# Kernel optimization log

Hardware: AMD Instinct MI355X
Metric: run time of the kernel (lower is better)

Reference implementation:

```python
import jax, jax.numpy as jnp
import numpy as np

B, D, H, W, C = 1, 16, 56, 56, 256
WD, WH, WW = 2, 7, 7
SD, SH, SW = 1, 3, 3
HEADS = 8
HDIM = C // HEADS
N = WD * WH * WW          # 98 tokens per window
NW = (D // WD) * (H // WH) * (W // WW)  # 512 windows per batch element
HID = 4 * C


def _rel_index():
    coords = np.stack(np.meshgrid(np.arange(WD), np.arange(WH), np.arange(WW), indexing='ij')).reshape(3, -1)
    rel = (coords[:, :, None] - coords[:, None, :]).transpose(1, 2, 0).astype(np.int64)
    rel[..., 0] += WD - 1; rel[..., 1] += WH - 1; rel[..., 2] += WW - 1
    rel[..., 0] *= (2 * WH - 1) * (2 * WW - 1)
    rel[..., 1] *= (2 * WW - 1)
    return rel.sum(-1)  # (N, N)

REL_INDEX = jnp.asarray(_rel_index())


def _np_window_partition(x):
    b, d, h, w, c = x.shape
    x = x.reshape(b, d // WD, WD, h // WH, WH, w // WW, WW, c)
    return x.transpose(0, 1, 3, 5, 2, 4, 6, 7).reshape(-1, N, c)


def _compute_mask():
    # Swin compute_mask: label 3x3x3 shifted regions, windows mask cross-region pairs with -100
    img = np.zeros((1, D, H, W, 1), np.float32)
    cnt = 0
    for ds in (slice(0, -WD), slice(-WD, -SD), slice(-SD, None)):
        for hs in (slice(0, -WH), slice(-WH, -SH), slice(-SH, None)):
            for ws in (slice(0, -WW), slice(-WW, -SW), slice(-SW, None)):
                img[:, ds, hs, ws, :] = cnt; cnt += 1
    mw = _np_window_partition(img).reshape(NW, N)
    am = mw[:, None, :] - mw[:, :, None]
    return np.where(am != 0, -100.0, 0.0).astype(np.float32)


def setup_inputs():
    key = jax.random.key(0)
    ks = jax.random.split(key, 8)
    s = 0.02
    return {
        'x': jax.random.normal(ks[0], (B, D, H, W, C), jnp.float32),
        'mask_matrix': jnp.asarray(_compute_mask()),
        'g1': jnp.ones((C,), jnp.float32), 'b1': jnp.zeros((C,), jnp.float32),
        'qkv_w': jax.random.normal(ks[1], (C, 3 * C), jnp.float32) * s,
        'qkv_b': jnp.zeros((3 * C,), jnp.float32),
        'rpb': jax.random.normal(ks[2], ((2 * WD - 1) * (2 * WH - 1) * (2 * WW - 1), HEADS), jnp.float32) * s,
        'proj_w': jax.random.normal(ks[3], (C, C), jnp.float32) * s,
        'proj_b': jnp.zeros((C,), jnp.float32),
        'g2': jnp.ones((C,), jnp.float32), 'b2': jnp.zeros((C,), jnp.float32),
        'fc1_w': jax.random.normal(ks[4], (C, HID), jnp.float32) * s,
        'fc1_b': jnp.zeros((HID,), jnp.float32),
        'fc2_w': jax.random.normal(ks[5], (HID, C), jnp.float32) * s,
        'fc2_b': jnp.zeros((C,), jnp.float32),
    }


def _ln(x, g, b):
    mu = jnp.mean(x, -1, keepdims=True)
    var = jnp.mean((x - mu) ** 2, -1, keepdims=True)
    return (x - mu) * jax.lax.rsqrt(var + 1e-5) * g + b


def _window_partition(x):
    b = x.shape[0]
    x = x.reshape(b, D // WD, WD, H // WH, WH, W // WW, WW, C)
    return x.transpose(0, 1, 3, 5, 2, 4, 6, 7).reshape(-1, N, C)


def _window_reverse(w):
    x = w.reshape(B, D // WD, H // WH, W // WW, WD, WH, WW, C)
    return x.transpose(0, 1, 4, 2, 5, 3, 6, 7).reshape(B, D, H, W, C)


def reference(x, mask_matrix, g1, b1, qkv_w, qkv_b, rpb, proj_w, proj_b, g2, b2, fc1_w, fc1_b, fc2_w, fc2_b):
    shortcut = x
    y = _ln(x, g1, b1)
    # D,H,W divide window sizes -> pad amounts are 0; cyclic shift for SW-MSA
    y = jnp.roll(y, shift=(-SD, -SH, -SW), axis=(1, 2, 3))
    xw = _window_partition(y)                          # (B_, N, C)
    B_ = xw.shape[0]
    qkv = (xw @ qkv_w + qkv_b).reshape(B_, N, 3, HEADS, HDIM)
    q, k, v = jnp.moveaxis(qkv, 2, 0)                  # each (B_, N, HEADS, HDIM)
    q = q * (HDIM ** -0.5)
    attn = jnp.einsum('bnhd,bmhd->bhnm', q, k)         # (B_, HEADS, N, N)
    bias = rpb[REL_INDEX.reshape(-1)].reshape(N, N, HEADS).transpose(2, 0, 1)
    attn = attn + bias[None]
    attn = attn.reshape(B_ // NW, NW, HEADS, N, N) + mask_matrix[None, :, None]
    attn = jax.nn.softmax(attn.reshape(B_, HEADS, N, N), axis=-1)
    out = jnp.einsum('bhnm,bmhd->bnhd', attn, v).reshape(B_, N, C)
    out = out @ proj_w + proj_b
    y = _window_reverse(out)
    y = jnp.roll(y, shift=(SD, SH, SW), axis=(1, 2, 3))
    x = shortcut + y
    h = _ln(x, g2, b2)
    h = jax.nn.gelu(h @ fc1_w + fc1_b, approximate=False)
    h = h @ fc2_w + fc2_b
    return x + h
```

## Files before the change

kernel.cpp:

```cpp
#include <hip/hip_runtime.h>
#include <hip/hip_bf16.h>

typedef __hip_bfloat16 bf16;
typedef __attribute__((ext_vector_type(4))) float f32x4;
typedef __attribute__((ext_vector_type(8))) short bf16x8;

#define MFMA16(a,b,c) __builtin_amdgcn_mfma_f32_16x16x32_bf16((a),(b),(c),0,0,0)

static __device__ inline unsigned short bfbits(float f) {
  __hip_bfloat16 h = __float2bfloat16(f);
  union { __hip_bfloat16 h; unsigned short u; } u;
  u.h = h; return u.u;
}
static __device__ inline float bf2f(unsigned short u) {
  return __uint_as_float(((unsigned int)u) << 16);
}
static __device__ inline void gld16(const void* g, void* l) {
  __builtin_amdgcn_global_load_lds((const __attribute__((address_space(1))) void*)g,
                                   (__attribute__((address_space(3))) void*)l, 16, 0, 0);
}

__global__ __launch_bounds__(256) void prep_k(const float* __restrict__ qkv_w,
                                              const float* __restrict__ proj_w,
                                              const float* __restrict__ fc1_w,
                                              const float* __restrict__ fc2_w,
                                              const float* __restrict__ rpb,
                                              bf16* __restrict__ wqkvT,
                                              bf16* __restrict__ wprojT,
                                              bf16* __restrict__ wfc1T,
                                              bf16* __restrict__ wfc2T,
                                              unsigned short* __restrict__ biasT,
                                              unsigned int* __restrict__ rowoff0,
                                              unsigned int* __restrict__ rowmap1) {
  const int b = blockIdx.x, tid = threadIdx.x;
  if (b < 768) {
    int idx = b * 256 + tid;
    int n = idx >> 8, k = idx & 255;
    float v = qkv_w[k * 768 + n];
    if (n < 256) v *= 0.17677669529663687f;
    wqkvT[idx] = __float2bfloat16(v);
  } else if (b < 1024) {
    int idx = (b - 768) * 256 + tid;
    int n = idx >> 8, k = idx & 255;
    wprojT[idx] = __float2bfloat16(proj_w[k * 256 + n]);
  } else if (b < 2048) {
    int idx = (b - 1024) * 256 + tid;
    int n = idx >> 8, k = idx & 255;
    wfc1T[idx] = __float2bfloat16(fc1_w[k * 1024 + n]);
  } else if (b < 3072) {
    int idx = (b - 2048) * 256 + tid;
    int n = idx >> 10, k = idx & 1023;
    wfc2T[idx] = __float2bfloat16(fc2_w[k * 256 + n]);
  } else if (b < 3110) {
    int idx = (b - 3072) * 256 + tid;
    if (idx < 9604) {
      int nn = idx / 98, mm = idx - nn * 98;
      int ld = nn / 49, lrem = nn - ld * 49, lh = lrem / 7, lw = lrem - lh * 7;
      int md = mm / 49, mrem = mm - md * 49, mh = mrem / 7, mw = mrem - mh * 7;
      int rel = (ld - md + 1) * 169 + (lh - mh + 6) * 13 + (lw - mw + 6);
      #pragma unroll
      for (int h = 0; h < 8; ++h)
        biasT[h * 9604 + mm * 98 + nn] = bfbits(rpb[rel * 8 + h]);
    }
  } else {
    int row = (b - 3110) * 256 + tid;
    if (row < 50176) {
      int widx = row / 98, n = row - widx * 98;
      rowoff0[row] = (unsigned int)(widx * 25088 + n * 32);
      int zd = widx >> 6, zh = (widx >> 3) & 7, zw = widx & 7;
      int ld = n / 49, rem = n - ld * 49, lh = rem / 7, lw = rem - lh * 7;
      int d = zd * 2 + ld, h = zh * 7 + lh, w = zw * 7 + lw;
      int dsrc = (d + 1) & 15;
      int hsrc = h + 3; if (hsrc >= 56) hsrc -= 56;
      int wsrc = w + 3; if (wsrc >= 56) wsrc -= 56;
      rowmap1[row] = (unsigned int)((dsrc * 56 + hsrc) * 56 + wsrc);
    }
  }
}

__global__ __launch_bounds__(256) void vtrans_k(const unsigned short* __restrict__ v,
                                                unsigned short* __restrict__ vt) {
  __shared__ unsigned short S[98 * 33];
  const unsigned short* src = v + (size_t)blockIdx.x * 3136;
  for (int i = threadIdx.x; i < 3136; i += 256) {
    int n = i >> 5, d = i & 31;
    S[n * 33 + d] = src[i];
  }
  __syncthreads();
  unsigned short* dst = vt + ((size_t)blockIdx.x << 12);
  for (int i = threadIdx.x; i < 4096; i += 256) {
    int d = i >> 7, m = i & 127;
    dst[i] = (m < 98) ? S[m * 33 + d] : (unsigned short)0;
  }
}

__global__ __launch_bounds__(256) void ln_k(const float* __restrict__ x,
                                            const float* __restrict__ g,
                                            const float* __restrict__ bias,
                                            bf16* __restrict__ out, int windowed) {
  const int wid = threadIdx.x >> 6, lane = threadIdx.x & 63;
  const int t = blockIdx.x * 4 + wid;
  int src = t;
  if (windowed) {
    int widx = t / 98, n = t - widx * 98;
    int zd = widx >> 6, zh = (widx >> 3) & 7, zw = widx & 7;
    int ld = n / 49, rem = n - ld * 49, lh = rem / 7, lw = rem - lh * 7;
    int d = zd * 2 + ld, h = zh * 7 + lh, w = zw * 7 + lw;
    int dsrc = (d + 1) & 15;
    int hsrc = h + 3; if (hsrc >= 56) hsrc -= 56;
    int wsrc = w + 3; if (wsrc >= 56) wsrc -= 56;
    src = (dsrc * 56 + hsrc) * 56 + wsrc;
  }
  const float4 v = *(const float4*)(x + (size_t)src * 256 + lane * 4);
  float s1 = v.x + v.y + v.z + v.w;
  float s2 = v.x * v.x + v.y * v.y + v.z * v.z + v.w * v.w;
  #pragma unroll
  for (int d = 1; d < 64; d <<= 1) {
    s1 += __shfl_xor(s1, d);
    s2 += __shfl_xor(s2, d);
  }
  float mu = s1 * (1.f / 256.f);
  float var = s2 * (1.f / 256.f) - mu * mu;
  float rs = rsqrtf(var + 1e-5f);
  const float4 gv = *(const float4*)(g + lane * 4);
  const float4 bv = *(const float4*)(bias + lane * 4);
  ushort4 pk;
  pk.x = bfbits((v.x - mu) * rs * gv.x + bv.x);
  pk.y = bfbits((v.y - mu) * rs * gv.y + bv.y);
  pk.z = bfbits((v.z - mu) * rs * gv.z + bv.z);
  pk.w = bfbits((v.w - mu) * rs * gv.w + bv.w);
  *(ushort4*)((unsigned short*)out + (size_t)t * 256 + lane * 4) = pk;
}

template<int EPI>
__global__ __launch_bounds__(512) void gemm_k(const bf16* __restrict__ A,
                                              const bf16* __restrict__ Bt,
                                              const float* __restrict__ bias,
                                              int N, int K, int NX, int mrow0,
                                              bf16* __restrict__ out_bf,
                                              float* __restrict__ out_f,
                                              const float* __restrict__ add_f,
                                              const unsigned int* __restrict__ rmap) {
  __shared__ bf16 As[2][128 * 32];
  __shared__ bf16 Bs[2][256 * 32];
  const int tid = threadIdx.x;
  const int wid = tid >> 6, lane = tid & 63;
  const int nwg = gridDim.x, xcd = blockIdx.x & 7, o8 = blockIdx.x >> 3;
  const int qq = nwg >> 3, r8 = nwg & 7;
  const int tile = (xcd < r8 ? xcd * (qq + 1) : r8 * (qq + 1) + (xcd - r8) * qq) + o8;
  const int bx = tile % NX, by = tile / NX;
  const int row0 = by * 128, col0 = bx * 256;
  const int fr = lane & 15, kh = lane >> 4;
  const int wm = (wid >> 2) * 64, wn = (wid & 3) * 64;
  f32x4 zero4 = {0.f, 0.f, 0.f, 0.f};
  f32x4 acc[4][4];
  #pragma unroll
  for (int i = 0; i < 4; ++i)
    #pragma unroll
    for (int j = 0; j < 4; ++j) acc[i][j] = zero4;

  const int srow = tid >> 2, sq = (tid & 3) * 8;
  const bf16* aP = A + (size_t)(row0 + srow) * K + sq;
  const bf16* bP = Bt + (size_t)(col0 + srow) * K + sq;
  const bf16* bP2 = Bt + (size_t)(col0 + srow + 128) * K + sq;
  bf16* asD = &As[0][srow * 32 + sq];
  bf16* bsD = &Bs[0][srow * 32 + sq];
  bf16* bsD2 = &Bs[0][(srow + 128) * 32 + sq];

  const int nk = K >> 5;
  gld16(aP, asD);
  gld16(bP, bsD);
  gld16(bP2, bsD2);

  int cur = 0;
  for (int t = 0; t < nk; ++t) {
    __syncthreads();
    if (t + 1 < nk) {
      int k0 = (t + 1) * 32;
      int so = (cur ^ 1);
      gld16(aP + k0, asD + so * 4096);
      gld16(bP + k0, bsD + so * 8192);
      gld16(bP2 + k0, bsD2 + so * 8192);
    }
    const bf16* Ab = As[cur];
    const bf16* Bb = Bs[cur];
    bf16x8 af[4], bfr[4];
    #pragma unroll
    for (int i = 0; i < 4; ++i)
      af[i] = *(const bf16x8*)&Ab[(wm + i * 16 + fr) * 32 + kh * 8];
    #pragma unroll
    for (int j = 0; j < 4; ++j)
      bfr[j] = *(const bf16x8*)&Bb[(wn + j * 16 + fr) * 32 + kh * 8];
    #pragma unroll
    for (int i = 0; i < 4; ++i)
      #pragma unroll
      for (int j = 0; j < 4; ++j)
        acc[i][j] = MFMA16(af[i], bfr[j], acc[i][j]);
    cur ^= 1;
  }

  #pragma unroll
  for (int i = 0; i < 4; ++i) {
    #pragma unroll
    for (int r = 0; r < 4; ++r) {
      int row = row0 + wm + i * 16 + kh * 4 + r;
      unsigned int rl = (EPI == 0 || EPI == 1) ? rmap[row] : 0u;
      #pragma unroll
      for (int j = 0; j < 4; ++j) {
        int col = col0 + wn + j * 16 + fr;
        float bb = bias[col];
        if (EPI == 0 && col < 256) bb *= 0.17677669529663687f;
        float v = acc[i][j][r] + bb;
        if (EPI == 0) {
          int part = col >> 8, head = (col >> 5) & 7, hd = col & 31;
          size_t off = (size_t)part * 12845056 + rl + head * 3136 + hd;
          out_bf[off] = __float2bfloat16(v);
        } else if (EPI == 1) {
          size_t tok = rl;
          out_f[tok * 256 + col] = add_f[tok * 256 + col] + v;
        } else if (EPI == 2) {
          float gl = 0.5f * v * (1.0f + erff(v * 0.70710678118654752f));
          out_bf[(size_t)row * 1024 + col] = __float2bfloat16(gl);
        } else {
          size_t ro = (size_t)(mrow0 + row);
          out_f[ro * 256 + col] = add_f[ro * 256 + col] + v;
        }
      }
    }
  }
}

__global__ __launch_bounds__(256, 2) void attn_k(const bf16* __restrict__ qkv,
                                                 const unsigned short* __restrict__ vt,
                                                 const unsigned short* __restrict__ bias_bf,
                                                 bf16* __restrict__ out) {
  __shared__ unsigned short Pl[112 * 128];
  __shared__ unsigned short biasS[112 * 100];
  __shared__ float invS[112];
  __shared__ unsigned char lblS[112];
  const int tid = threadIdx.x;
  const int widx = blockIdx.x >> 1, hh = blockIdx.x & 1;
  const int wid = tid >> 6, lane = tid & 63;
  const int fr = lane & 15, kh = lane >> 4, kh4 = kh * 4;
  const int tr0 = wid * 2;
  f32x4 zero4 = {0.f, 0.f, 0.f, 0.f};

  if (tid < 112) {
    unsigned char l = 255;
    if (tid < 98) {
      int zd = widx >> 6, zh = (widx >> 3) & 7, zw = widx & 7;
      int ld = tid / 49, rem = tid - ld * 49, lh = rem / 7, lw = rem - lh * 7;
      int d = zd * 2 + ld, h = zh * 7 + lh, w = zw * 7 + lw;
      int cd = (d >= 14) + (d >= 15);
      int ch = (h >= 49) + (h >= 53);
      int cw = (w >= 49) + (w >= 53);
      l = (unsigned char)(cd * 9 + ch * 3 + cw);
    }
    lblS[tid] = l;
  }
  __syncthreads();

  unsigned int lblK[7];
  #pragma unroll
  for (int mt = 0; mt < 7; ++mt)
    lblK[mt] = *(const unsigned int*)&lblS[mt * 16 + kh4];
  const bool t1v = (tr0 + 1) < 7;
  unsigned int lq0 = 0x01010101u * lblS[tr0 * 16 + fr];
  unsigned int lq1 = 0x01010101u * lblS[(t1v ? tr0 + 1 : 0) * 16 + fr];

  for (int it = 0; it < 4; ++it) {
    const int head = hh * 4 + it;
    const unsigned short* qbu = (const unsigned short*)qkv + ((size_t)widx * 8 + head) * 3136;
    const unsigned short* kbu = qbu + (size_t)12845056;
    const unsigned short* brow = bias_bf + head * 9604;
    const unsigned short* vtb = vt + (((size_t)widx * 8 + head) << 12);

    __syncthreads();
    for (int j = tid; j < 4802; j += 256) {
      int n = j / 49, m2 = (j - n * 49) * 2;
      *(unsigned int*)&biasS[n * 100 + m2] = *(const unsigned int*)(brow + n * 98 + m2);
    }
    for (int j = tid; j < 700; j += 256) {
      int n = j / 50, m2 = (j - n * 50) * 2;
      *(unsigned int*)&biasS[(98 + n) * 100 + m2] = 0xFF80FF80u;
    }

    int qr0 = tr0 * 16 + fr; if (qr0 > 97) qr0 = 97;
    int qr1 = (tr0 + 1) * 16 + fr; if (qr1 > 97) qr1 = 97;
    bf16x8 aq0 = *(const bf16x8*)(qbu + qr0 * 32 + kh * 8);
    bf16x8 aq1 = *(const bf16x8*)(qbu + qr1 * 32 + kh * 8);

    f32x4 s2[2][7];
    #pragma unroll
    for (int a = 0; a < 2; ++a)
      #pragma unroll
      for (int m = 0; m < 7; ++m) s2[a][m] = zero4;
    #pragma unroll
    for (int mt = 0; mt < 7; ++mt) {
      int krow = mt * 16 + fr; if (krow > 97) krow = 97;
      bf16x8 kf = *(const bf16x8*)(kbu + krow * 32 + kh * 8);
      s2[0][mt] = MFMA16(kf, aq0, s2[0][mt]);
      s2[1][mt] = MFMA16(kf, aq1, s2[1][mt]);
    }
    __syncthreads();

    #pragma unroll
    for (int ti = 0; ti < 2; ++ti) {
      int tr = tr0 + ti;
      if (tr < 7) {
        int q = tr * 16 + fr;
        int qc = (q < 98) ? q : 0;
        unsigned int lq = (ti == 0) ? lq0 : lq1;
        float mxa = -1e30f, mxb = -1e30f;
        #pragma unroll
        for (int mt = 0; mt < 7; ++mt) {
          unsigned int df = lblK[mt] ^ lq;
          #pragma unroll
          for (int r = 0; r < 4; ++r) {
            int k = mt * 16 + kh4 + r;
            float b = bf2f(biasS[k * 100 + qc]);
            float msk = ((df >> (8 * r)) & 255u) ? -100.f : 0.f;
            s2[ti][mt][r] = s2[ti][mt][r] + b + msk;
          }
          mxa = fmaxf(mxa, fmaxf(s2[ti][mt][0], s2[ti][mt][1]));
          mxb = fmaxf(mxb, fmaxf(s2[ti][mt][2], s2[ti][mt][3]));
        }
        float mx = fmaxf(mxa, mxb);
        mx = fmaxf(mx, __shfl_xor(mx, 16));
        mx = fmaxf(mx, __shfl_xor(mx, 32));
        float suma = 0.f, sumb = 0.f;
        #pragma unroll
        for (int mt = 0; mt < 7; ++mt) {
          float e0 = __expf(s2[ti][mt][0] - mx);
          float e1 = __expf(s2[ti][mt][1] - mx);
          float e2 = __expf(s2[ti][mt][2] - mx);
          float e3 = __expf(s2[ti][mt][3] - mx);
          s2[ti][mt][0] = e0; s2[ti][mt][1] = e1;
          s2[ti][mt][2] = e2; s2[ti][mt][3] = e3;
          suma += e0 + e1; sumb += e2 + e3;
        }
        float sum = suma + sumb;
        sum += __shfl_xor(sum, 16);
        sum += __shfl_xor(sum, 32);
        if (kh == 0) invS[q] = 1.0f / sum;
        #pragma unroll
        for (int mt = 0; mt < 7; ++mt) {
          ushort4 pk;
          pk.x = bfbits(s2[ti][mt][0]);
          pk.y = bfbits(s2[ti][mt][1]);
          pk.z = bfbits(s2[ti][mt][2]);
          pk.w = bfbits(s2[ti][mt][3]);
          *(ushort4*)&Pl[(q * 128 + mt * 16 + kh4) ^ ((q & 7) << 3)] = pk;
        }
        ushort4 zz; zz.x = zz.y = zz.z = zz.w = 0;
        *(ushort4*)&Pl[(q * 128 + 112 + kh4) ^ ((q & 7) << 3)] = zz;
      }
    }

    f32x4 o00 = zero4, o01 = zero4, o10 = zero4, o11 = zero4;
    #pragma unroll
    for (int kk = 0; kk < 4; ++kk) {
      bf16x8 vv0 = *(const bf16x8*)(vtb + fr * 128 + kk * 32 + kh * 8);
      bf16x8 vv1 = *(const bf16x8*)(vtb + (16 + fr) * 128 + kk * 32 + kh * 8);
      int prow0 = tr0 * 16 + fr;
      bf16x8 pa0 = *(const bf16x8*)&((const bf16*)Pl)[(prow0 * 128 + kk * 32 + kh * 8) ^ ((prow0 & 7) << 3)];
      o00 = MFMA16(pa0, vv0, o00);
      o01 = MFMA16(pa0, vv1, o01);
      if (t1v) {
        int prow1 = prow0 + 16;
        bf16x8 pa1 = *(const bf16x8*)&((const bf16*)Pl)[(prow1 * 128 + kk * 32 + kh * 8) ^ ((prow1 & 7) << 3)];
        o10 = MFMA16(pa1, vv0, o10);
        o11 = MFMA16(pa1, vv1, o11);
      }
    }
    #pragma unroll
    for (int r = 0; r < 4; ++r) {
      int row = tr0 * 16 + kh4 + r;
      if (row < 98) {
        float iv = invS[row];
        size_t grow = (size_t)widx * 98 + row;
        out[grow * 256 + head * 32 + fr] = __float2bfloat16(o00[r] * iv);
        out[grow * 256 + head * 32 + 16 + fr] = __float2bfloat16(o01[r] * iv);
      }
    }
    if (t1v) {
      #pragma unroll
      for (int r = 0; r < 4; ++r) {
        int row = (tr0 + 1) * 16 + kh4 + r;
        if (row < 98) {
          float iv = invS[row];
          size_t grow = (size_t)widx * 98 + row;
          out[grow * 256 + head * 32 + fr] = __float2bfloat16(o10[r] * iv);
          out[grow * 256 + head * 32 + 16 + fr] = __float2bfloat16(o11[r] * iv);
        }
      }
    }
  }
}

extern "C" void kernel_launch(void* const* d_in, const int* in_sizes, int n_in,
                              void* d_out, int out_size, void* d_ws, size_t ws_size,
                              hipStream_t stream) {
  const float* x      = (const float*)d_in[0];
  const float* g1     = (const float*)d_in[2];
  const float* b1     = (const float*)d_in[3];
  const float* qkv_w  = (const float*)d_in[4];
  const float* qkv_b  = (const float*)d_in[5];
  const float* rpb    = (const float*)d_in[6];
  const float* proj_w = (const float*)d_in[7];
  const float* proj_b = (const float*)d_in[8];
  const float* g2     = (const float*)d_in[9];
  const float* b2     = (const float*)d_in[10];
  const float* fc1_w  = (const float*)d_in[11];
  const float* fc1_b  = (const float*)d_in[12];
  const float* fc2_w  = (const float*)d_in[13];
  const float* fc2_b  = (const float*)d_in[14];
  float* outp = (float*)d_out;

  char* ws = (char*)d_ws;
  if (ws_size < (size_t)156237824) return;
  bf16*  wqkvT   = (bf16*)(ws + 0);
  bf16*  wprojT  = (bf16*)(ws + 393216);
  bf16*  wfc1T   = (bf16*)(ws + 524288);
  bf16*  wfc2T   = (bf16*)(ws + 1048576);
  unsigned short* bias_bf = (unsigned short*)(ws + 1572864);
  unsigned int* rowmap1 = (unsigned int*)(ws + 1726528);
  float* x2      = (float*)(ws + 2097152);
  unsigned int* rowoff0 = (unsigned int*)(ws + 2097152);
  unsigned short* vtb = (unsigned short*)(ws + 11931648);
  char*  pool    = ws + 53477376;
  bf16*  xw       = (bf16*)pool;
  bf16*  qkvb     = (bf16*)(pool + 25690112);
  bf16*  attn_out = (bf16*)pool;
  bf16*  hbuf     = (bf16*)pool;
  bf16*  hh       = (bf16*)(pool + 25690112);

  prep_k<<<3307, 256, 0, stream>>>(qkv_w, proj_w, fc1_w, fc2_w, rpb,
                                   wqkvT, wprojT, wfc1T, wfc2T, bias_bf,
                                   rowoff0, rowmap1);

  ln_k<<<12544, 256, 0, stream>>>(x, g1, b1, xw, 1);
  gemm_k<0><<<1176, 512, 0, stream>>>(xw, wqkvT, qkv_b, 768, 256, 3, 0,
                                      qkvb, nullptr, nullptr, rowoff0);
  vtrans_k<<<4096, 256, 0, stream>>>((const unsigned short*)qkvb + (size_t)2 * 12845056, vtb);
  attn_k<<<1024, 256, 0, stream>>>(qkvb, vtb, bias_bf, attn_out);
  gemm_k<1><<<392, 512, 0, stream>>>(attn_out, wprojT, proj_b, 256, 256, 1, 0,
                                     nullptr, x2, x, rowmap1);
  ln_k<<<12544, 256, 0, stream>>>(x2, g2, b2, hbuf, 0);
  for (int ch = 0; ch < 2; ++ch) {
    gemm_k<2><<<784, 512, 0, stream>>>(hbuf + (size_t)ch * 25088 * 256, wfc1T, fc1_b,
                                       1024, 256, 4, 0, hh, nullptr, nullptr, nullptr);
    gemm_k<3><<<196, 512, 0, stream>>>(hh, wfc2T, fc2_b, 256, 1024, 1, ch * 25088,
                                       nullptr, outp, x2, nullptr);
  }
}
```

Baseline: 307.1 us.

## Fuse MLP fc1+GELU+fc2 into one kernel keeping hidden tile in LDS

```diff
diff --git a/kernel.cpp b/kernel.cpp
--- a/kernel.cpp
+++ b/kernel.cpp
@@ -203,7 +203,7 @@
   for (int i = 0; i < 4; ++i) {
     #pragma unroll
     for (int r = 0; r < 4; ++r) {
-      int row = row0 + wm + i * 16 + kh * 4 + r;
+      int row = row0 + wm + i * 16 + (lane >> 4) * 4 + r;
       unsigned int rl = (EPI == 0 || EPI == 1) ? rmap[row] : 0u;
       #pragma unroll
       for (int j = 0; j < 4; ++j) {
@@ -218,13 +218,126 @@
         } else if (EPI == 1) {
           size_t tok = rl;
           out_f[tok * 256 + col] = add_f[tok * 256 + col] + v;
-        } else if (EPI == 2) {
+        }
+      }
+    }
+  }
+}
+
+__global__ __launch_bounds__(256) void mlp_k(const bf16* __restrict__ hbuf,
+                                             const bf16* __restrict__ w1,
+                                             const bf16* __restrict__ w2,
+                                             const float* __restrict__ b1,
+                                             const float* __restrict__ b2,
+                                             const float* __restrict__ x2,
+                                             float* __restrict__ out) {
+  __shared__ bf16 Ah[64 * 256];
+  __shared__ bf16 Hh[64 * 256];
+  const int tid = threadIdx.x;
+  const int wid = tid >> 6, lane = tid & 63;
+  const int fr = lane & 15, kh = lane >> 4, kh4 = kh * 4;
+  const int wn = wid * 64;
+  const int row0 = blockIdx.x * 64;
+  f32x4 zero4 = {0.f, 0.f, 0.f, 0.f};
+
+  {
+    int row = tid >> 2, cg = (tid & 3) * 64;
+    const bf16* src = hbuf + (size_t)(row0 + row) * 256 + cg;
+    #pragma unroll
+    for (int c = 0; c < 8; ++c) {
+      bf16x8 v = *(const bf16x8*)(src + c * 8);
+      *(bf16x8*)&Ah[(row * 256 + cg + c * 8) ^ ((row & 7) << 3)] = v;
+    }
+  }
+  __syncthreads();
+
+  f32x4 acc2[4][4];
+  #pragma unroll
+  for (int i = 0; i < 4; ++i)
+    #pragma unroll
+    for (int j = 0; j < 4; ++j) acc2[i][j] = zero4;
+
+  for (int p = 0; p < 4; ++p) {
+    f32x4 acc1[4][4];
+    #pragma unroll
+    for (int i = 0; i < 4; ++i)
+      #pragma unroll
+      for (int j = 0; j < 4; ++j) acc1[i][j] = zero4;
+    const bf16* w1p = w1 + (size_t)(p * 256 + wn) * 256;
+    bf16x8 bcur[4], bnxt[4];
+    #pragma unroll
+    for (int j = 0; j < 4; ++j)
+      bcur[j] = *(const bf16x8*)(w1p + (j * 16 + fr) * 256 + kh * 8);
+    #pragma unroll
+    for (int t = 0; t < 8; ++t) {
+      if (t < 7) {
+        #pragma unroll
+        for (int j = 0; j < 4; ++j)
+          bnxt[j] = *(const bf16x8*)(w1p + (j * 16 + fr) * 256 + (t + 1) * 32 + kh * 8);
+      }
+      bf16x8 af[4];
+      #pragma unroll
+      for (int i = 0; i < 4; ++i)
+        af[i] = *(const bf16x8*)&Ah[((i * 16 + fr) * 256 + t * 32 + kh * 8) ^ ((fr & 7) << 3)];
+      #pragma unroll
+      for (int i = 0; i < 4; ++i)
+        #pragma unroll
+        for (int j = 0; j < 4; ++j)
+          acc1[i][j] = MFMA16(af[i], bcur[j], acc1[i][j]);
+      #pragma unroll
+      for (int j = 0; j < 4; ++j) bcur[j] = bnxt[j];
+    }
+    __syncthreads();
+    #pragma unroll
+    for (int j = 0; j < 4; ++j) {
+      float b1v = b1[p * 256 + wn + j * 16 + fr];
+      #pragma unroll
+      for (int i = 0; i < 4; ++i) {
+        #pragma unroll
+        for (int r = 0; r < 4; ++r) {
+          float v = acc1[i][j][r] + b1v;
           float gl = 0.5f * v * (1.0f + erff(v * 0.70710678118654752f));
-          out_bf[(size_t)row * 1024 + col] = __float2bfloat16(gl);
-        } else {
-          size_t ro = (size_t)(mrow0 + row);
-          out_f[ro * 256 + col] = add_f[ro * 256 + col] + v;
+          int row = i * 16 + kh4 + r;
+          Hh[(row * 256 + wn + j * 16 + fr) ^ ((row & 7) << 3)] = __float2bfloat16(gl);
         }
+      }
+    }
+    __syncthreads();
+    const bf16* w2p = w2 + p * 256;
+    bf16x8 c2[4], n2[4];
+    #pragma unroll
+    for (int j = 0; j < 4; ++j)
+      c2[j] = *(const bf16x8*)(w2p + (size_t)(wn + j * 16 + fr) * 1024 + kh * 8);
+    #pragma unroll
+    for (int t = 0; t < 8; ++t) {
+      if (t < 7) {
+        #pragma unroll
+        for (int j = 0; j < 4; ++j)
+          n2[j] = *(const bf16x8*)(w2p + (size_t)(wn + j * 16 + fr) * 1024 + (t + 1) * 32 + kh * 8);
+      }
+      bf16x8 hf[4];
+      #pragma unroll
+      for (int i = 0; i < 4; ++i)
+        hf[i] = *(const bf16x8*)&Hh[((i * 16 + fr) * 256 + t * 32 + kh * 8) ^ ((fr & 7) << 3)];
+      #pragma unroll
+      for (int i = 0; i < 4; ++i)
+        #pragma unroll
+        for (int j = 0; j < 4; ++j)
+          acc2[i][j] = MFMA16(hf[i], c2[j], acc2[i][j]);
+      #pragma unroll
+      for (int j = 0; j < 4; ++j) c2[j] = n2[j];
+    }
+  }
+
+  #pragma unroll
+  for (int i = 0; i < 4; ++i) {
+    #pragma unroll
+    for (int r = 0; r < 4; ++r) {
+      size_t row = (size_t)row0 + i * 16 + kh4 + r;
+      #pragma unroll
+      for (int j = 0; j < 4; ++j) {
+        int col = wn + j * 16 + fr;
+        out[row * 256 + col] = x2[row * 256 + col] + acc2[i][j][r] + b2[col];
       }
     }
   }
@@ -433,7 +546,6 @@
   bf16*  qkvb     = (bf16*)(pool + 25690112);
   bf16*  attn_out = (bf16*)pool;
   bf16*  hbuf     = (bf16*)pool;
-  bf16*  hh       = (bf16*)(pool + 25690112);
 
   prep_k<<<3307, 256, 0, stream>>>(qkv_w, proj_w, fc1_w, fc2_w, rpb,
                                    wqkvT, wprojT, wfc1T, wfc2T, bias_bf,
@@ -447,10 +559,5 @@
   gemm_k<1><<<392, 512, 0, stream>>>(attn_out, wprojT, proj_b, 256, 256, 1, 0,
                                      nullptr, x2, x, rowmap1);
   ln_k<<<12544, 256, 0, stream>>>(x2, g2, b2, hbuf, 0);
-  for (int ch = 0; ch < 2; ++ch) {
-    gemm_k<2><<<784, 512, 0, stream>>>(hbuf + (size_t)ch * 25088 * 256, wfc1T, fc1_b,
-                                       1024, 256, 4, 0, hh, nullptr, nullptr, nullptr);
-    gemm_k<3><<<196, 512, 0, stream>>>(hh, wfc2T, fc2_b, 256, 1024, 1, ch * 25088,
-                                       nullptr, outp, x2, nullptr);
-  }
-}
+  mlp_k<<<784, 256, 0, stream>>>(hbuf, wfc1T, wfc2T, fc1_b, fc2_b, x2, outp);
+}
```

Result: slower. 382.8 us (+24.6%).
